# Kernel tuning notes

Measured on AMD Instinct MI355X. Metric: run time of the kernel, lower is better.

## Reference

```python
import jax, jax.numpy as jnp
import numpy as np

INIT_STDEV = 0.01

def setup_inputs() -> dict:
    key = jax.random.key(0)
    k1, k2, k3 = jax.random.split(key, 3)
    B, S, D = 8, 4096, 768
    x = jax.random.normal(k1, (B, S, D), dtype=jnp.float32)
    att_v = jax.random.normal(k2, (D,), dtype=jnp.float32) * INIT_STDEV
    att_W = jax.random.normal(k3, (D, D), dtype=jnp.float32) * INIT_STDEV
    return {"x": x, "att_v": att_v, "att_W": att_W}

def reference(x, att_v, att_W):
    # y = x @ W : [B,S,D]; scores = tanh(y) . v over D : [B,S]
    y = jnp.tanh(jnp.einsum('bsd,de->bse', x, att_W))
    scores = jnp.einsum('bsd,d->bs', y, att_v)
    weights = jax.nn.softmax(scores, axis=-1)            # softmax over sequence
    out = jnp.einsum('bs,bsd->bd', weights, x)           # attsum pool
    return out.astype(jnp.float32)
```

## Files before the change

kernel.cpp:

```cpp
#include <hip/hip_runtime.h>
#include <hip/hip_bf16.h>

constexpr int Bb = 8;
constexpr int Ss = 4096;
constexpr int Dd = 768;
constexpr int Mm = Bb * Ss;

typedef __bf16 bf16x8 __attribute__((ext_vector_type(8)));
typedef __bf16 bf16x4 __attribute__((ext_vector_type(4)));
typedef float f32x4 __attribute__((ext_vector_type(4)));

__device__ __forceinline__ float fast_tanh(float x) {
    return 1.f - 2.f / (__expf(2.f * x) + 1.f);
}

__device__ __forceinline__ void load_lds16(const void* g, void* l) {
    __builtin_amdgcn_global_load_lds(
        (const __attribute__((address_space(1))) unsigned int*)g,
        (__attribute__((address_space(3))) unsigned int*)l, 16, 0, 0);
}

__global__ __launch_bounds__(256) void convW(const float* __restrict__ W,
                                             __bf16* __restrict__ Wt) {
    __shared__ float tile[32][33];
    const int tx = threadIdx.x & 31;
    const int ty = threadIdx.x >> 5;
    const int kb = blockIdx.x * 32;
    const int nb = blockIdx.y * 32;
#pragma unroll
    for (int i = 0; i < 32; i += 8)
        tile[ty + i][tx] = W[(size_t)(kb + ty + i) * Dd + nb + tx];
    __syncthreads();
#pragma unroll
    for (int i = 0; i < 32; i += 8)
        Wt[(size_t)(nb + ty + i) * Dd + kb + tx] = (__bf16)tile[tx][ty + i];
}

__global__ __launch_bounds__(512, 4) void scores_gemm(
    const float* __restrict__ x, const __bf16* __restrict__ Wt,
    const float* __restrict__ v, float* __restrict__ scores) {
    __shared__ __bf16 As[2][64 * 32];
    __shared__ __bf16 Bs[2][384 * 32];
    __shared__ float ssc[8][32];

    const int t = threadIdx.x;
    const int nb = blockIdx.x;
    const int mb = blockIdx.y;
    const int lane = t & 63;
    const int wave = t >> 6;
    const int wm = wave >> 2;
    const int wn = wave & 3;
    const int quad = lane >> 4;
    const int lid = lane & 15;

    const int arow = t >> 3;
    const int ac4 = t & 7;
    const float* agp = x + (size_t)(mb * 64 + arow) * Dd + ac4 * 4;

    const __bf16* bg[3];
    int bl[3];
#pragma unroll
    for (int j = 0; j < 3; ++j) {
        const int flat = j * 8192 + t * 16;
        const int col = flat >> 6;
        const int off = flat & 63;
        bg[j] = Wt + (size_t)(nb * 384 + col) * Dd + (off >> 1);
        bl[j] = flat >> 1;
    }

    f32x4 acc[2][6];
#pragma unroll
    for (int tm = 0; tm < 2; ++tm)
#pragma unroll
        for (int nt = 0; nt < 6; ++nt) acc[tm][nt] = (f32x4){0.f, 0.f, 0.f, 0.f};

    {
        const float4 a = *(const float4*)(agp);
        bf16x4 p;
        p[0] = (__bf16)a.x; p[1] = (__bf16)a.y; p[2] = (__bf16)a.z; p[3] = (__bf16)a.w;
        *(bf16x4*)(&As[0][arow * 32 + ac4 * 4]) = p;
#pragma unroll
        for (int j = 0; j < 3; ++j) load_lds16(bg[j], &Bs[0][bl[j]]);
    }

    for (int kb = 0; kb < 24; ++kb) {
        const int p = kb & 1;
        __syncthreads();

        float4 an;
        if (kb < 23) {
            an = *(const float4*)(agp + (kb + 1) * 32);
#pragma unroll
            for (int j = 0; j < 3; ++j)
                load_lds16(bg[j] + (kb + 1) * 32, &Bs[1 - p][bl[j]]);
        }

        bf16x8 af[2], bfr[6];
#pragma unroll
        for (int tm = 0; tm < 2; ++tm)
            af[tm] = *(const bf16x8*)(&As[p][(wm * 32 + tm * 16 + lid) * 32 + quad * 8]);
#pragma unroll
        for (int nt = 0; nt < 6; ++nt)
            bfr[nt] = *(const bf16x8*)(&Bs[p][(wn * 96 + nt * 16 + lid) * 32 + quad * 8]);

#pragma unroll
        for (int tm = 0; tm < 2; ++tm)
#pragma unroll
            for (int nt = 0; nt < 6; ++nt)
                acc[tm][nt] = __builtin_amdgcn_mfma_f32_16x16x32_bf16(af[tm], bfr[nt], acc[tm][nt], 0, 0, 0);

        if (kb < 23) {
            bf16x4 pa;
            pa[0] = (__bf16)an.x; pa[1] = (__bf16)an.y;
            pa[2] = (__bf16)an.z; pa[3] = (__bf16)an.w;
            *(bf16x4*)(&As[1 - p][arow * 32 + ac4 * 4]) = pa;
        }
    }

    float vv[6];
#pragma unroll
    for (int nt = 0; nt < 6; ++nt)
        vv[nt] = v[nb * 384 + wn * 96 + nt * 16 + lid];

#pragma unroll
    for (int tm = 0; tm < 2; ++tm)
#pragma unroll
        for (int r = 0; r < 4; ++r) {
            float s = 0.f;
#pragma unroll
            for (int nt = 0; nt < 6; ++nt) s += vv[nt] * fast_tanh(acc[tm][nt][r]);
            s += __shfl_xor(s, 1);
            s += __shfl_xor(s, 2);
            s += __shfl_xor(s, 4);
            s += __shfl_xor(s, 8);
            if (lid == 0) ssc[wave][tm * 16 + quad * 4 + r] = s;
        }
    __syncthreads();
    if (t < 64) {
        const int wmh = t >> 5;
        const int rl = t & 31;
        float s = 0.f;
#pragma unroll
        for (int ww = 0; ww < 4; ++ww) s += ssc[wmh * 4 + ww][rl];
        atomicAdd(&scores[mb * 64 + t], s);
    }
}

__global__ __launch_bounds__(256) void softmax_k(const float* __restrict__ scores,
                                                 float* __restrict__ weights) {
    const int b = blockIdx.x;
    const int t = threadIdx.x;
    const float* s = scores + (size_t)b * Ss;
    float* wgt = weights + (size_t)b * Ss;
    __shared__ float red[256];

    float mx = -1e30f;
    for (int i = t; i < Ss; i += 256) mx = fmaxf(mx, s[i]);
    red[t] = mx;
    __syncthreads();
    for (int o = 128; o > 0; o >>= 1) {
        if (t < o) red[t] = fmaxf(red[t], red[t + o]);
        __syncthreads();
    }
    mx = red[0];
    __syncthreads();
    float sum = 0.f;
    for (int i = t; i < Ss; i += 256) {
        const float e = __expf(s[i] - mx);
        wgt[i] = e;
        sum += e;
    }
    red[t] = sum;
    __syncthreads();
    for (int o = 128; o > 0; o >>= 1) {
        if (t < o) red[t] += red[t + o];
        __syncthreads();
    }
    const float inv = 1.f / red[0];
    for (int i = t; i < Ss; i += 256) wgt[i] *= inv;
}

__global__ __launch_bounds__(192) void pool1(const float* __restrict__ x,
                                             const float* __restrict__ weights,
                                             float* __restrict__ partial) {
    const int b = blockIdx.y;
    const int c = blockIdx.x;
    const int t = threadIdx.x;
    const float* base = x + ((size_t)b * Ss + c * 32) * Dd;
    const float* wrow = weights + (size_t)b * Ss + c * 32;
    float4 acc = make_float4(0.f, 0.f, 0.f, 0.f);
#pragma unroll 8
    for (int i = 0; i < 32; ++i) {
        const float ww = wrow[i];
        const float4 xv = *(const float4*)(base + (size_t)i * Dd + t * 4);
        acc.x += ww * xv.x;
        acc.y += ww * xv.y;
        acc.z += ww * xv.z;
        acc.w += ww * xv.w;
    }
    *(float4*)(partial + ((size_t)(b * 128 + c)) * Dd + t * 4) = acc;
}

__global__ __launch_bounds__(768) void pool2(const float* __restrict__ partial,
                                             float* __restrict__ out) {
    const int b = blockIdx.x;
    const int d = threadIdx.x;
    float s = 0.f;
#pragma unroll 8
    for (int c = 0; c < 128; ++c) s += partial[((size_t)(b * 128 + c)) * Dd + d];
    out[(size_t)b * Dd + d] = s;
}

extern "C" void kernel_launch(void* const* d_in, const int* in_sizes, int n_in,
                              void* d_out, int out_size, void* d_ws, size_t ws_size,
                              hipStream_t stream) {
    (void)in_sizes; (void)n_in; (void)ws_size; (void)out_size;
    const float* x = (const float*)d_in[0];
    const float* v = (const float*)d_in[1];
    const float* W = (const float*)d_in[2];

    char* ws = (char*)d_ws;
    __bf16* Wt = (__bf16*)ws;
    float* scores = (float*)(ws + 1179648);
    float* weights = (float*)(ws + 1179648 + 131072);
    float* partial = (float*)(ws + 1179648 + 262144);

    hipMemsetAsync(scores, 0, Mm * sizeof(float), stream);

    convW<<<dim3(Dd / 32, Dd / 32), 256, 0, stream>>>(W, Wt);
    scores_gemm<<<dim3(2, Mm / 64), 512, 0, stream>>>(x, Wt, v, scores);
    softmax_k<<<dim3(Bb), 256, 0, stream>>>(scores, weights);
    pool1<<<dim3(128, Bb), 192, 0, stream>>>(x, weights, partial);
    pool2<<<dim3(Bb), 768, 0, stream>>>(partial, (float*)d_out);
}
```

Baseline: 240.8 us.

## Load A fragments directly to registers, triple-buffer B, swizzle LDS, drop atomics

The GEMM kernel stops staging x through LDS. Each lane loads its A fragment straight from global memory into registers and converts it to bf16 there. B tiles are triple-buffered with explicit vmcnt waits and raw barriers, so loads are issued two steps ahead. Wt is written in an XOR-swizzled layout to avoid LDS bank conflicts, and blocks are remapped so that concurrently running blocks share x rows. The two N-halves now write separate score arrays instead of using atomics plus a memset, and the softmax normalisation moves into pool2 as a single scale. The hand-written waitcnt counts are fragile, and redundant A global loads across the four wn waves add traffic.

```diff
diff --git a/kernel.cpp b/kernel.cpp
--- a/kernel.cpp
+++ b/kernel.cpp
@@ -7,7 +7,6 @@
 constexpr int Mm = Bb * Ss;
 
 typedef __bf16 bf16x8 __attribute__((ext_vector_type(8)));
-typedef __bf16 bf16x4 __attribute__((ext_vector_type(4)));
 typedef float f32x4 __attribute__((ext_vector_type(4)));
 
 __device__ __forceinline__ float fast_tanh(float x) {
@@ -32,30 +31,34 @@
         tile[ty + i][tx] = W[(size_t)(kb + ty + i) * Dd + nb + tx];
     __syncthreads();
 #pragma unroll
-    for (int i = 0; i < 32; i += 8)
-        Wt[(size_t)(nb + ty + i) * Dd + kb + tx] = (__bf16)tile[tx][ty + i];
+    for (int i = 0; i < 32; i += 8) {
+        const int n = nb + ty + i;
+        const int txs = (tx & 7) | ((((tx >> 3) & 3) ^ ((n >> 1) & 3)) << 3);
+        Wt[(size_t)n * Dd + kb + txs] = (__bf16)tile[tx][ty + i];
+    }
 }
 
 __global__ __launch_bounds__(512, 4) void scores_gemm(
     const float* __restrict__ x, const __bf16* __restrict__ Wt,
-    const float* __restrict__ v, float* __restrict__ scores) {
-    __shared__ __bf16 As[2][64 * 32];
-    __shared__ __bf16 Bs[2][384 * 32];
+    const float* __restrict__ v, float* __restrict__ scores2) {
+    __shared__ __bf16 Bs[3][384 * 32];
     __shared__ float ssc[8][32];
 
     const int t = threadIdx.x;
-    const int nb = blockIdx.x;
-    const int mb = blockIdx.y;
+    const int id = blockIdx.x;
+    const int ids = ((id & 7) * 128) + (id >> 3);
+    const int mb = ids >> 1;
+    const int nb = ids & 1;
     const int lane = t & 63;
     const int wave = t >> 6;
     const int wm = wave >> 2;
     const int wn = wave & 3;
     const int quad = lane >> 4;
     const int lid = lane & 15;
-
-    const int arow = t >> 3;
-    const int ac4 = t & 7;
-    const float* agp = x + (size_t)(mb * 64 + arow) * Dd + ac4 * 4;
+    const int rslot = ((quad ^ ((lid >> 1) & 3)) * 8);
+
+    const float* ag0 = x + (size_t)(mb * 64 + wm * 32 + lid) * Dd + quad * 8;
+    const float* ag1 = ag0 + (size_t)16 * Dd;
 
     const __bf16* bg[3];
     int bl[3];
@@ -63,8 +66,7 @@
     for (int j = 0; j < 3; ++j) {
         const int flat = j * 8192 + t * 16;
         const int col = flat >> 6;
-        const int off = flat & 63;
-        bg[j] = Wt + (size_t)(nb * 384 + col) * Dd + (off >> 1);
+        bg[j] = Wt + (size_t)(nb * 384 + col) * Dd + ((flat & 63) >> 1);
         bl[j] = flat >> 1;
     }
 
@@ -74,47 +76,56 @@
 #pragma unroll
         for (int nt = 0; nt < 6; ++nt) acc[tm][nt] = (f32x4){0.f, 0.f, 0.f, 0.f};
 
-    {
-        const float4 a = *(const float4*)(agp);
-        bf16x4 p;
-        p[0] = (__bf16)a.x; p[1] = (__bf16)a.y; p[2] = (__bf16)a.z; p[3] = (__bf16)a.w;
-        *(bf16x4*)(&As[0][arow * 32 + ac4 * 4]) = p;
-#pragma unroll
-        for (int j = 0; j < 3; ++j) load_lds16(bg[j], &Bs[0][bl[j]]);
-    }
-
-    for (int kb = 0; kb < 24; ++kb) {
-        const int p = kb & 1;
-        __syncthreads();
-
-        float4 an;
-        if (kb < 23) {
-            an = *(const float4*)(agp + (kb + 1) * 32);
+    float4 ap0a, ap0b, ap1a, ap1b;
+#pragma unroll
+    for (int j = 0; j < 3; ++j) load_lds16(bg[j], &Bs[0][bl[j]]);
+    ap0a = *(const float4*)(ag0);
+    ap0b = *(const float4*)(ag0 + 4);
+    ap1a = *(const float4*)(ag1);
+    ap1b = *(const float4*)(ag1 + 4);
+#pragma unroll
+    for (int j = 0; j < 3; ++j) load_lds16(bg[j] + 32, &Bs[1][bl[j]]);
+
+#pragma unroll
+    for (int k = 0; k < 24; ++k) {
+        if (k == 23) asm volatile("s_waitcnt vmcnt(4)" ::: "memory");
+        else         asm volatile("s_waitcnt vmcnt(7)" ::: "memory");
+        __builtin_amdgcn_sched_barrier(0);
+        __builtin_amdgcn_s_barrier();
+        __builtin_amdgcn_sched_barrier(0);
+
+        bf16x8 af0, af1;
+        af0[0] = (__bf16)ap0a.x; af0[1] = (__bf16)ap0a.y;
+        af0[2] = (__bf16)ap0a.z; af0[3] = (__bf16)ap0a.w;
+        af0[4] = (__bf16)ap0b.x; af0[5] = (__bf16)ap0b.y;
+        af0[6] = (__bf16)ap0b.z; af0[7] = (__bf16)ap0b.w;
+        af1[0] = (__bf16)ap1a.x; af1[1] = (__bf16)ap1a.y;
+        af1[2] = (__bf16)ap1a.z; af1[3] = (__bf16)ap1a.w;
+        af1[4] = (__bf16)ap1b.x; af1[5] = (__bf16)ap1b.y;
+        af1[6] = (__bf16)ap1b.z; af1[7] = (__bf16)ap1b.w;
+
+        if (k < 23) {
+            ap0a = *(const float4*)(ag0 + (k + 1) * 32);
+            ap0b = *(const float4*)(ag0 + (k + 1) * 32 + 4);
+            ap1a = *(const float4*)(ag1 + (k + 1) * 32);
+            ap1b = *(const float4*)(ag1 + (k + 1) * 32 + 4);
+        }
+        if (k < 22) {
 #pragma unroll
             for (int j = 0; j < 3; ++j)
-                load_lds16(bg[j] + (kb + 1) * 32, &Bs[1 - p][bl[j]]);
-        }
-
-        bf16x8 af[2], bfr[6];
-#pragma unroll
-        for (int tm = 0; tm < 2; ++tm)
-            af[tm] = *(const bf16x8*)(&As[p][(wm * 32 + tm * 16 + lid) * 32 + quad * 8]);
-#pragma unroll
-        for (int nt = 0; nt < 6; ++nt)
-            bfr[nt] = *(const bf16x8*)(&Bs[p][(wn * 96 + nt * 16 + lid) * 32 + quad * 8]);
-
-#pragma unroll
-        for (int tm = 0; tm < 2; ++tm)
-#pragma unroll
-            for (int nt = 0; nt < 6; ++nt)
-                acc[tm][nt] = __builtin_amdgcn_mfma_f32_16x16x32_bf16(af[tm], bfr[nt], acc[tm][nt], 0, 0, 0);
-
-        if (kb < 23) {
-            bf16x4 pa;
-            pa[0] = (__bf16)an.x; pa[1] = (__bf16)an.y;
-            pa[2] = (__bf16)an.z; pa[3] = (__bf16)an.w;
-            *(bf16x4*)(&As[1 - p][arow * 32 + ac4 * 4]) = pa;
-        }
+                load_lds16(bg[j] + (k + 2) * 32, &Bs[(k + 2) % 3][bl[j]]);
+        }
+        __builtin_amdgcn_sched_barrier(0);
+
+        const __bf16* bsp = &Bs[k % 3][(wn * 96 + lid) * 32 + rslot];
+        __builtin_amdgcn_s_setprio(1);
+#pragma unroll
+        for (int nt = 0; nt < 6; ++nt) {
+            const bf16x8 bfr = *(const bf16x8*)(bsp + nt * 512);
+            acc[0][nt] = __builtin_amdgcn_mfma_f32_16x16x32_bf16(af0, bfr, acc[0][nt], 0, 0, 0);
+            acc[1][nt] = __builtin_amdgcn_mfma_f32_16x16x32_bf16(af1, bfr, acc[1][nt], 0, 0, 0);
+        }
+        __builtin_amdgcn_s_setprio(0);
     }
 
     float vv[6];
@@ -142,20 +153,26 @@
         float s = 0.f;
 #pragma unroll
         for (int ww = 0; ww < 4; ++ww) s += ssc[wmh * 4 + ww][rl];
-        atomicAdd(&scores[mb * 64 + t], s);
-    }
-}
-
-__global__ __launch_bounds__(256) void softmax_k(const float* __restrict__ scores,
-                                                 float* __restrict__ weights) {
+        scores2[(size_t)nb * Mm + mb * 64 + t] = s;
+    }
+}
+
+__global__ __launch_bounds__(256) void softmax_k(const float* __restrict__ scores2,
+                                                 float* __restrict__ weights,
+                                                 float* __restrict__ sinv) {
     const int b = blockIdx.x;
     const int t = threadIdx.x;
-    const float* s = scores + (size_t)b * Ss;
+    const float* s0 = scores2 + (size_t)b * Ss;
+    const float* s1 = s0 + Mm;
     float* wgt = weights + (size_t)b * Ss;
     __shared__ float red[256];
 
     float mx = -1e30f;
-    for (int i = t; i < Ss; i += 256) mx = fmaxf(mx, s[i]);
+    for (int i = t; i < Ss; i += 256) {
+        const float sc = s0[i] + s1[i];
+        wgt[i] = sc;
+        mx = fmaxf(mx, sc);
+    }
     red[t] = mx;
     __syncthreads();
     for (int o = 128; o > 0; o >>= 1) {
@@ -166,7 +183,7 @@
     __syncthreads();
     float sum = 0.f;
     for (int i = t; i < Ss; i += 256) {
-        const float e = __expf(s[i] - mx);
+        const float e = __expf(wgt[i] - mx);
         wgt[i] = e;
         sum += e;
     }
@@ -176,8 +193,7 @@
         if (t < o) red[t] += red[t + o];
         __syncthreads();
     }
-    const float inv = 1.f / red[0];
-    for (int i = t; i < Ss; i += 256) wgt[i] *= inv;
+    if (t == 0) sinv[b] = 1.f / red[0];
 }
 
 __global__ __launch_bounds__(192) void pool1(const float* __restrict__ x,
@@ -202,13 +218,14 @@
 }
 
 __global__ __launch_bounds__(768) void pool2(const float* __restrict__ partial,
+                                             const float* __restrict__ sinv,
                                              float* __restrict__ out) {
     const int b = blockIdx.x;
     const int d = threadIdx.x;
     float s = 0.f;
 #pragma unroll 8
     for (int c = 0; c < 128; ++c) s += partial[((size_t)(b * 128 + c)) * Dd + d];
-    out[(size_t)b * Dd + d] = s;
+    out[(size_t)b * Dd + d] = s * sinv[b];
 }
 
 extern "C" void kernel_launch(void* const* d_in, const int* in_sizes, int n_in,
@@ -221,15 +238,14 @@
 
     char* ws = (char*)d_ws;
     __bf16* Wt = (__bf16*)ws;
-    float* scores = (float*)(ws + 1179648);
-    float* weights = (float*)(ws + 1179648 + 131072);
-    float* partial = (float*)(ws + 1179648 + 262144);
-
-    hipMemsetAsync(scores, 0, Mm * sizeof(float), stream);
+    float* scores2 = (float*)(ws + 1179648);
+    float* weights = (float*)(ws + 1179648 + 262144);
+    float* sinv    = (float*)(ws + 1179648 + 262144 + 131072);
+    float* partial = (float*)(ws + 1179648 + 262144 + 131072 + 32);
 
     convW<<<dim3(Dd / 32, Dd / 32), 256, 0, stream>>>(W, Wt);
-    scores_gemm<<<dim3(2, Mm / 64), 512, 0, stream>>>(x, Wt, v, scores);
-    softmax_k<<<dim3(Bb), 256, 0, stream>>>(scores, weights);
+    scores_gemm<<<dim3(2 * Mm / 64), 512, 0, stream>>>(x, Wt, v, scores2);
+    softmax_k<<<dim3(Bb), 256, 0, stream>>>(scores2, weights, sinv);
     pool1<<<dim3(128, Bb), 192, 0, stream>>>(x, weights, partial);
-    pool2<<<dim3(Bb), 768, 0, stream>>>(partial, (float*)d_out);
-}
+    pool2<<<dim3(Bb), 768, 0, stream>>>(partial, sinv, (float*)d_out);
+}
```

Measured after the change: 324.6 us. 1.35x slower.
